# Kernel tuning notes

Measured on AMD Instinct MI355X. Metric: run time of the kernel, lower is better.

The kernel has to match this reference:

```python
import jax, jax.numpy as jnp
import numpy as np

TEMPERATURE = 0.1


def setup_inputs() -> dict:
    key = jax.random.key(0)
    # Scale by 0.03 so exp((z/T)@(z/T).T) stays finite in fp32 (module uses
    # an unstabilized exp-sum-log, and the diagonal is ||z||^2 / T^2).
    z = jax.random.normal(key, (16384, 128), dtype=jnp.float32) * 0.03
    return {"z": z}


def reference(z) -> jnp.ndarray:
    n = z.shape[0]
    zs = z / TEMPERATURE                      # [N, d]
    a = zs @ zs.T                             # [N, N] self-similarity
    # Faithful to the original: -log(sum(exp(a), axis=1) / N), then mean.
    l = -jnp.log(jnp.exp(a).sum(axis=1) / n)  # [N]
    return l.mean()
```

## Files before the change

### kernel.cpp

```cpp
#include <hip/hip_runtime.h>
#include <stdint.h>

#define NROW 16384
#define DDIM 128
#define ROWB 256

constexpr int NB     = 64;
constexpr int NJT    = NROW / NB;
constexpr int CHUNK  = 8;
constexpr int NSTRIP = 128;
constexpr int NBLK   = 2112;

typedef __bf16 bf16x8 __attribute__((ext_vector_type(8)));
typedef float  f32x4  __attribute__((ext_vector_type(4)));
typedef int    i32x4  __attribute__((ext_vector_type(4)));

typedef const uint32_t __attribute__((address_space(1)))* gptr_t;
typedef uint32_t __attribute__((address_space(3)))*       lptr_t;

__device__ __forceinline__ unsigned short f2bf(float x) {
  union { float f; uint32_t u; } c; c.f = x;
  uint32_t u = c.u + 0x7fffu + ((c.u >> 16) & 1u);
  return (unsigned short)(u >> 16);
}

__device__ __forceinline__ int Sfun(int k) {
  const int q = k >> 2, r = k & 3;
  return 2 * q * (q + 1) + r * (q + 1);
}

__global__ __launch_bounds__(256) void prep_kernel(const float* __restrict__ z,
                                                   unsigned short* __restrict__ zs,
                                                   float* __restrict__ s) {
  const float SC = 12.011224087864498f;
  int t = blockIdx.x * 256 + threadIdx.x;
  float4 v = reinterpret_cast<const float4*>(z)[t];
  ushort4 o;
  o.x = f2bf(v.x * SC); o.y = f2bf(v.y * SC);
  o.z = f2bf(v.z * SC); o.w = f2bf(v.w * SC);
  reinterpret_cast<ushort4*>(zs)[t] = o;
  if (t < NROW) s[t] = 0.0f;
}

__global__ __launch_bounds__(256, 2) void gemm_exp_kernel(const unsigned short* __restrict__ zs,
                                                          float* __restrict__ s) {
  __shared__ __align__(16) char smem[2 * NB * ROWB + 4 * CHUNK * 64 * 4];
  float* csm = (float*)(smem + 2 * NB * ROWB);
  const int tid  = threadIdx.x;
  const int lane = tid & 63;
  const int wid  = tid >> 6;

  int I, c;
  {
    const int bid = blockIdx.x;
    const int m = NBLK - bid;
    int k = (int)sqrtf(8.0f * (float)m);
    if (k > 128) k = 128;
    while (Sfun(k) < m) ++k;
    while (k > 1 && Sfun(k - 1) >= m) --k;
    I = 128 - k;
    c = bid - (NBLK - Sfun(k));
  }
  const int mI     = NJT - 2 * I;
  const int jt0    = 2 * I + CHUNK * c;
  const int JT_blk = min(CHUNK, mI - CHUNK * c);

  const int rowBase = I * 128 + wid * 32;
  const char* zb = (const char*)zs;
  const int kb = (lane >> 4) << 4;

  bf16x8 afrag[2][4];
  {
    const int r0 = rowBase + (lane & 15);
#pragma unroll
    for (int mf = 0; mf < 2; ++mf)
#pragma unroll
      for (int ks = 0; ks < 4; ++ks) {
        i32x4 raw = *reinterpret_cast<const i32x4*>(
            zb + (size_t)(r0 + mf * 16) * ROWB + ks * 64 + kb);
        afrag[mf][ks] = __builtin_bit_cast(bf16x8, raw);
      }
  }

  float rs[2][4];
  float cs[4];
#pragma unroll
  for (int mf = 0; mf < 2; ++mf)
#pragma unroll
    for (int r = 0; r < 4; ++r) rs[mf][r] = 0.0f;
#pragma unroll
  for (int nf = 0; nf < 4; ++nf) cs[nf] = 0.0f;

#define STAGE_B(buf, k)                                                          \
  {                                                                              \
    _Pragma("unroll")                                                            \
    for (int i_ = 0; i_ < 4; ++i_) {                                             \
      const int destByte_ = wid * 4096 + i_ * 1024 + lane * 16;                  \
      const int r_  = destByte_ >> 8;                                            \
      const int cb_ = destByte_ & 0xF0;                                          \
      const int srcByte_ = ((jt0 + (k)) * NB + r_) * ROWB                        \
                           + (cb_ ^ ((r_ & 7) << 4));                            \
      __builtin_amdgcn_global_load_lds((gptr_t)(zb + srcByte_),                  \
          (lptr_t)(smem + (buf) * (NB * ROWB) + destByte_), 16, 0, 0);           \
    }                                                                            \
  }

  STAGE_B(0, 0);

#pragma unroll 1
  for (int k = 0; k < JT_blk; ++k) {
    const int cur = k & 1;
    if (k + 1 < JT_blk) {
      STAGE_B(cur ^ 1, k + 1);
      asm volatile("s_waitcnt vmcnt(4)" ::: "memory");
    } else {
      asm volatile("s_waitcnt vmcnt(0)" ::: "memory");
    }
    __builtin_amdgcn_s_barrier();

    f32x4 acc[2][4];
#pragma unroll
    for (int mf = 0; mf < 2; ++mf)
#pragma unroll
      for (int nf = 0; nf < 4; ++nf) {
        f32x4 zv = {0.f, 0.f, 0.f, 0.f};
        acc[mf][nf] = zv;
      }

    const char* bufp = smem + cur * (NB * ROWB);
#pragma unroll
    for (int ks = 0; ks < 4; ++ks) {
      bf16x8 bfrag[4];
#pragma unroll
      for (int nf = 0; nf < 4; ++nf) {
        const int r   = nf * 16 + (lane & 15);
        const int kk  = ks * 64 + kb;
        const int off = r * ROWB + (kk ^ ((r & 7) << 4));
        i32x4 raw = *reinterpret_cast<const i32x4*>(bufp + off);
        bfrag[nf] = __builtin_bit_cast(bf16x8, raw);
      }
#pragma unroll
      for (int mf = 0; mf < 2; ++mf)
#pragma unroll
        for (int nf = 0; nf < 4; ++nf)
          acc[mf][nf] = __builtin_amdgcn_mfma_f32_16x16x32_bf16(
              afrag[mf][ks], bfrag[nf], acc[mf][nf], 0, 0, 0);
    }

#pragma unroll
    for (int mf = 0; mf < 2; ++mf)
#pragma unroll
      for (int nf = 0; nf < 4; ++nf) {
        f32x4 a4 = acc[mf][nf];
        float e0 = __builtin_amdgcn_exp2f(a4[0]);
        float e1 = __builtin_amdgcn_exp2f(a4[1]);
        float e2 = __builtin_amdgcn_exp2f(a4[2]);
        float e3 = __builtin_amdgcn_exp2f(a4[3]);
        rs[mf][0] += e0; rs[mf][1] += e1; rs[mf][2] += e2; rs[mf][3] += e3;
        cs[nf] += (e0 + e1) + (e2 + e3);
      }

#pragma unroll
    for (int nf = 0; nf < 4; ++nf) {
      float v = cs[nf];
      v += __shfl_xor(v, 16);
      v += __shfl_xor(v, 32);
      if (lane < 16) csm[wid * (CHUNK * 64) + k * 64 + nf * 16 + lane] = v;
      cs[nf] = 0.0f;
    }

    __builtin_amdgcn_s_barrier();
  }
#undef STAGE_B

#pragma unroll
  for (int mf = 0; mf < 2; ++mf)
#pragma unroll
    for (int r = 0; r < 4; ++r) {
      float v = rs[mf][r];
      v += __shfl_xor(v, 1);
      v += __shfl_xor(v, 2);
      v += __shfl_xor(v, 4);
      v += __shfl_xor(v, 8);
      if ((lane & 15) == 0) {
        const int row = rowBase + mf * 16 + ((lane >> 4) << 2) + r;
        atomicAdd(&s[row], v);
      }
    }

  __syncthreads();
  {
    const int colBase0 = jt0 * NB;
    const int diagEnd  = (I + 1) * 128;
    const int ncol     = JT_blk * NB;
#pragma unroll
    for (int k4 = 0; k4 < 2; ++k4) {
      const int idx = k4 * 256 + tid;
      if (idx < ncol) {
        const int col = colBase0 + idx;
        if (col >= diagEnd) {
          float sum = csm[idx] + csm[CHUNK * 64 + idx]
                    + csm[2 * CHUNK * 64 + idx] + csm[3 * CHUNK * 64 + idx];
          atomicAdd(&s[col], sum);
        }
      }
    }
  }
}

__global__ __launch_bounds__(1024) void reduce_kernel(const float* __restrict__ s,
                                                      float* __restrict__ out) {
  const int tid = threadIdx.x;
  float acc = 0.0f;
  for (int i = tid; i < NROW; i += 1024) acc += __log2f(s[i]);
#pragma unroll
  for (int m = 32; m >= 1; m >>= 1) acc += __shfl_xor(acc, m);
  __shared__ float wsum[16];
  if ((tid & 63) == 0) wsum[tid >> 6] = acc;
  __syncthreads();
  if (tid == 0) {
    float tot = 0.0f;
#pragma unroll
    for (int w = 0; w < 16; ++w) tot += wsum[w];
    out[0] = logf((float)NROW) - 0.6931471805599453f * tot / (float)NROW;
  }
}

extern "C" void kernel_launch(void* const* d_in, const int* in_sizes, int n_in,
                              void* d_out, int out_size, void* d_ws, size_t ws_size,
                              hipStream_t stream) {
  const float* z = (const float*)d_in[0];
  unsigned short* zs = (unsigned short*)d_ws;
  float* s = (float*)((char*)d_ws + (size_t)NROW * DDIM * 2);
  float* out = (float*)d_out;

  prep_kernel<<<dim3(NROW * DDIM / 4 / 256), dim3(256), 0, stream>>>(z, zs, s);
  gemm_exp_kernel<<<dim3(NBLK), dim3(256), 0, stream>>>(zs, s);
  reduce_kernel<<<dim3(1), dim3(1024), 0, stream>>>(s, out);
}
```

Baseline: 66.96 us.

## Triple-buffer B tiles, double chunk size, and accumulate column sums via LDS atomics

Doubles the column tiles per block from 8 to 16, which halves the grid and reworks the triangular block-index mapping. The B staging moves from a double buffer to a triple buffer with prefetch distance two, which drops the second barrier per iteration. Per-wave column-sum slots are replaced by one shared LDS array updated with atomic adds. This aims to cut barrier, launch and global-atomic overhead and hide load latency better. In exchange it uses more LDS per block, which may lower occupancy, and adds LDS atomic contention.

```diff
diff --git a/kernel.cpp b/kernel.cpp
--- a/kernel.cpp
+++ b/kernel.cpp
@@ -7,9 +7,9 @@
 
 constexpr int NB     = 64;
 constexpr int NJT    = NROW / NB;
-constexpr int CHUNK  = 8;
+constexpr int CHUNK  = 16;
 constexpr int NSTRIP = 128;
-constexpr int NBLK   = 2112;
+constexpr int NBLK   = 1088;
 
 typedef __bf16 bf16x8 __attribute__((ext_vector_type(8)));
 typedef float  f32x4  __attribute__((ext_vector_type(4)));
@@ -24,9 +24,9 @@
   return (unsigned short)(u >> 16);
 }
 
-__device__ __forceinline__ int Sfun(int k) {
-  const int q = k >> 2, r = k & 3;
-  return 2 * q * (q + 1) + r * (q + 1);
+__device__ __forceinline__ int Tfun(int k) {
+  const int q = k >> 3, r = k & 7;
+  return 4 * q * (q + 1) + r * (q + 1);
 }
 
 __global__ __launch_bounds__(256) void prep_kernel(const float* __restrict__ z,
@@ -44,8 +44,8 @@
 
 __global__ __launch_bounds__(256, 2) void gemm_exp_kernel(const unsigned short* __restrict__ zs,
                                                           float* __restrict__ s) {
-  __shared__ __align__(16) char smem[2 * NB * ROWB + 4 * CHUNK * 64 * 4];
-  float* csm = (float*)(smem + 2 * NB * ROWB);
+  __shared__ __align__(16) char smem[3 * NB * ROWB + CHUNK * 64 * 4];
+  float* csm = (float*)(smem + 3 * NB * ROWB);
   const int tid  = threadIdx.x;
   const int lane = tid & 63;
   const int wid  = tid >> 6;
@@ -54,12 +54,13 @@
   {
     const int bid = blockIdx.x;
     const int m = NBLK - bid;
-    int k = (int)sqrtf(8.0f * (float)m);
+    int k = (int)sqrtf(16.0f * (float)m);
     if (k > 128) k = 128;
-    while (Sfun(k) < m) ++k;
-    while (k > 1 && Sfun(k - 1) >= m) --k;
+    if (k < 1) k = 1;
+    while (Tfun(k) < m) ++k;
+    while (k > 1 && Tfun(k - 1) >= m) --k;
     I = 128 - k;
-    c = bid - (NBLK - Sfun(k));
+    c = bid - (NBLK - Tfun(k));
   }
   const int mI     = NJT - 2 * I;
   const int jt0    = 2 * I + CHUNK * c;
@@ -68,28 +69,6 @@
   const int rowBase = I * 128 + wid * 32;
   const char* zb = (const char*)zs;
   const int kb = (lane >> 4) << 4;
-
-  bf16x8 afrag[2][4];
-  {
-    const int r0 = rowBase + (lane & 15);
-#pragma unroll
-    for (int mf = 0; mf < 2; ++mf)
-#pragma unroll
-      for (int ks = 0; ks < 4; ++ks) {
-        i32x4 raw = *reinterpret_cast<const i32x4*>(
-            zb + (size_t)(r0 + mf * 16) * ROWB + ks * 64 + kb);
-        afrag[mf][ks] = __builtin_bit_cast(bf16x8, raw);
-      }
-  }
-
-  float rs[2][4];
-  float cs[4];
-#pragma unroll
-  for (int mf = 0; mf < 2; ++mf)
-#pragma unroll
-    for (int r = 0; r < 4; ++r) rs[mf][r] = 0.0f;
-#pragma unroll
-  for (int nf = 0; nf < 4; ++nf) cs[nf] = 0.0f;
 
 #define STAGE_B(buf, k)                                                          \
   {                                                                              \
@@ -106,17 +85,47 @@
   }
 
   STAGE_B(0, 0);
-
+  if (JT_blk > 1) STAGE_B(1, 1);
+
+  bf16x8 afrag[2][4];
+  {
+    const int r0 = rowBase + (lane & 15);
+#pragma unroll
+    for (int mf = 0; mf < 2; ++mf)
+#pragma unroll
+      for (int ks = 0; ks < 4; ++ks) {
+        i32x4 raw = *reinterpret_cast<const i32x4*>(
+            zb + (size_t)(r0 + mf * 16) * ROWB + ks * 64 + kb);
+        afrag[mf][ks] = __builtin_bit_cast(bf16x8, raw);
+      }
+  }
+
+  f32x4 rsv[2];
+  float cs[4];
+  rsv[0] = (f32x4){0.f, 0.f, 0.f, 0.f};
+  rsv[1] = (f32x4){0.f, 0.f, 0.f, 0.f};
+#pragma unroll
+  for (int nf = 0; nf < 4; ++nf) cs[nf] = 0.0f;
+
+#pragma unroll
+  for (int q = 0; q < CHUNK * 64 / 256; ++q) csm[q * 256 + tid] = 0.0f;
+  asm volatile("s_waitcnt lgkmcnt(0)" ::: "memory");
+  __builtin_amdgcn_s_barrier();
+
+  int cur = 0;
 #pragma unroll 1
   for (int k = 0; k < JT_blk; ++k) {
-    const int cur = k & 1;
     if (k + 1 < JT_blk) {
-      STAGE_B(cur ^ 1, k + 1);
       asm volatile("s_waitcnt vmcnt(4)" ::: "memory");
     } else {
       asm volatile("s_waitcnt vmcnt(0)" ::: "memory");
     }
     __builtin_amdgcn_s_barrier();
+
+    if (k + 2 < JT_blk) {
+      int stg = cur - 1; if (stg < 0) stg += 3;
+      STAGE_B(stg, k + 2);
+    }
 
     f32x4 acc[2][4];
 #pragma unroll
@@ -152,12 +161,13 @@
 #pragma unroll
       for (int nf = 0; nf < 4; ++nf) {
         f32x4 a4 = acc[mf][nf];
-        float e0 = __builtin_amdgcn_exp2f(a4[0]);
-        float e1 = __builtin_amdgcn_exp2f(a4[1]);
-        float e2 = __builtin_amdgcn_exp2f(a4[2]);
-        float e3 = __builtin_amdgcn_exp2f(a4[3]);
-        rs[mf][0] += e0; rs[mf][1] += e1; rs[mf][2] += e2; rs[mf][3] += e3;
-        cs[nf] += (e0 + e1) + (e2 + e3);
+        f32x4 ev;
+        ev[0] = __builtin_amdgcn_exp2f(a4[0]);
+        ev[1] = __builtin_amdgcn_exp2f(a4[1]);
+        ev[2] = __builtin_amdgcn_exp2f(a4[2]);
+        ev[3] = __builtin_amdgcn_exp2f(a4[3]);
+        rsv[mf] += ev;
+        cs[nf] += (ev[0] + ev[1]) + (ev[2] + ev[3]);
       }
 
 #pragma unroll
@@ -165,11 +175,11 @@
       float v = cs[nf];
       v += __shfl_xor(v, 16);
       v += __shfl_xor(v, 32);
-      if (lane < 16) csm[wid * (CHUNK * 64) + k * 64 + nf * 16 + lane] = v;
+      if (lane < 16) atomicAdd(&csm[k * 64 + nf * 16 + lane], v);
       cs[nf] = 0.0f;
     }
 
-    __builtin_amdgcn_s_barrier();
+    ++cur; if (cur == 3) cur = 0;
   }
 #undef STAGE_B
 
@@ -177,7 +187,7 @@
   for (int mf = 0; mf < 2; ++mf)
 #pragma unroll
     for (int r = 0; r < 4; ++r) {
-      float v = rs[mf][r];
+      float v = rsv[mf][r];
       v += __shfl_xor(v, 1);
       v += __shfl_xor(v, 2);
       v += __shfl_xor(v, 4);
@@ -194,15 +204,11 @@
     const int diagEnd  = (I + 1) * 128;
     const int ncol     = JT_blk * NB;
 #pragma unroll
-    for (int k4 = 0; k4 < 2; ++k4) {
+    for (int k4 = 0; k4 < 4; ++k4) {
       const int idx = k4 * 256 + tid;
       if (idx < ncol) {
         const int col = colBase0 + idx;
-        if (col >= diagEnd) {
-          float sum = csm[idx] + csm[CHUNK * 64 + idx]
-                    + csm[2 * CHUNK * 64 + idx] + csm[3 * CHUNK * 64 + idx];
-          atomicAdd(&s[col], sum);
-        }
+        if (col >= diagEnd) atomicAdd(&s[col], csm[idx]);
       }
     }
   }
```

Result: slower. 97.51 us (+45.6%).
